# Kernel tuning notes

Hardware: AMD Instinct MI355X
Metric: run time of the kernel (lower is better)

Reference implementation:

```python
import jax, jax.numpy as jnp
import numpy as np
from jax.scipy.linalg import expm

CUTOFF = 8   # Fock cutoff D
M = 4        # qumodes
L = 2        # CVNeuralNet layers
N_OUT = 4
B = 4096     # batch
TWO_PI = 2.0 * np.pi

_n = jnp.arange(CUTOFF, dtype=jnp.float32)                      # number basis
_A = jnp.diag(jnp.sqrt(_n[1:]), 1).astype(jnp.complex64)        # annihilation op
_AD = _A.conj().T
_I = jnp.eye(CUTOFF, dtype=jnp.complex64)
_a1 = jnp.kron(_A, _I)   # mode-1 annihilation on 2-mode space
_a2 = jnp.kron(_I, _A)   # mode-2 annihilation on 2-mode space


def _disp(alpha):
    """Displacement gate D(alpha) = expm(alpha a^ - alpha* a) on truncated Fock space."""
    alpha = jnp.asarray(alpha, jnp.complex64)
    return expm(alpha * _AD - jnp.conj(alpha) * _A)


def _squeeze(r, phi):
    """Squeezing gate S(z) = expm((z* a^2 - z a^\u20202)/2), z = r e^{i phi}."""
    z = r * jnp.exp(1j * phi)
    return expm(0.5 * (jnp.conj(z) * (_A @ _A) - z * (_AD @ _AD)))


def _bs(theta, phi):
    """Beamsplitter BS(theta, phi) = expm(theta (e^{i phi} a1 a2^ - e^{-i phi} a1^ a2))."""
    H = theta * (jnp.exp(1j * phi) * _a1 @ _a2.conj().T - jnp.exp(-1j * phi) * _a1.conj().T @ _a2)
    return expm(H).reshape(CUTOFF, CUTOFF, CUTOFF, CUTOFF)


def _apply1(state, G, mode):
    # state: [B, D, D, D, D]; G: [D, D] acting on `mode`
    st = jnp.moveaxis(state, 1 + mode, -1)
    st = st @ G.T
    return jnp.moveaxis(st, -1, 1 + mode)


def _apply2(state, G, m1, m2):
    # G: [D, D, D, D] = (out1, out2, in1, in2)
    st = jnp.moveaxis(state, (1 + m1, 1 + m2), (-2, -1))
    st = jnp.einsum('ijkl,bxykl->bxyij', G, st.reshape(st.shape[0], -1, CUTOFF, CUTOFF, CUTOFF).reshape(st.shape)) if False else jnp.einsum('ijkl,b...kl->b...ij', G, st)
    return jnp.moveaxis(st, (-2, -1), (1 + m1, 1 + m2))


def _apply_diag(state, d, mode):
    shape = [1] * (M + 1)
    shape[1 + mode] = CUTOFF
    return state * d.reshape(shape)


def _interferometer(state, theta, phi, varphi):
    # PennyLane rectangular mesh: BS on (k, k+1) when (l + k) % 2 != 1, then rotations
    idx = 0
    for l in range(M):
        for k in range(M - 1):
            if (l + k) % 2 != 1:
                state = _apply2(state, _bs(theta[idx], phi[idx]), k, k + 1)
                idx += 1
    for m in range(M):
        state = _apply_diag(state, jnp.exp(1j * varphi[m] * _n), m)
    return state


def _forward(x, theta1, phi1, varphi1, r, phi_r, theta2, phi2, varphi2, a_amp, phi_a, kappa):
    # Displacement embedding: |psi0> = prod_m D(x_m)|0>, i.e. outer product of first columns
    Gs = jax.vmap(_disp)(x.reshape(-1)).reshape(x.shape[0], M, CUTOFF, CUTOFF)
    cols = Gs[..., 0]  # [B, M, D] : D(alpha)|0>
    state = jnp.einsum('bi,bj,bk,bl->bijkl', cols[:, 0], cols[:, 1], cols[:, 2], cols[:, 3])
    for l in range(L):
        state = _interferometer(state, theta1[l], phi1[l], varphi1[l])
        for m in range(M):
            state = _apply1(state, _squeeze(r[l, m], phi_r[l, m]), m)
        state = _interferometer(state, theta2[l], phi2[l], varphi2[l])
        for m in range(M):
            state = _apply1(state, _disp(a_amp[l, m] * jnp.exp(1j * phi_a[l, m])), m)
        for m in range(M):  # Kerr: diag exp(i kappa n^2)
            state = _apply_diag(state, jnp.exp(1j * kappa[l, m] * _n ** 2), m)
    # <X_i> = <a_i + a_i^> = 2 Re <psi| a_i |psi>  (hbar = 2 SF convention)
    outs = []
    for i in range(N_OUT):
        a_psi = _apply1(state, _A, i)
        exp_a = jnp.sum(jnp.conj(state) * a_psi, axis=tuple(range(1, M + 1)))
        outs.append(2.0 * jnp.real(exp_a))
    return jnp.stack(outs, axis=-1)  # [B, N_OUT]


def setup_inputs() -> dict:
    key = jax.random.key(0)
    ks = jax.random.split(key, 10)
    Kp = M * (M - 1) // 2
    u = lambda k, shape: jax.random.uniform(k, shape, jnp.float32, 0.0, TWO_PI)
    return {
        'x': jax.random.uniform(ks[0], (B, M), jnp.float32) * 0.5,
        'theta1': u(ks[1], (L, Kp)), 'phi1': u(ks[2], (L, Kp)), 'varphi1': u(ks[3], (L, M)),
        'r': jnp.full((L, M), 0.1, jnp.float32), 'phi_r': u(ks[4], (L, M)),
        'theta2': u(ks[5], (L, Kp)), 'phi2': u(ks[6], (L, Kp)), 'varphi2': u(ks[7], (L, M)),
        'a_amp': jnp.full((L, M), 0.1, jnp.float32), 'phi_a': u(ks[8], (L, M)),
        'kappa': u(ks[9], (L, M)),
    }


def reference(x, theta1, phi1, varphi1, r, phi_r, theta2, phi2, varphi2, a_amp, phi_a, kappa):
    return _forward(x, theta1, phi1, varphi1, r, phi_r, theta2, phi2, varphi2, a_amp, phi_a, kappa)
```

## Files before the change

### kernel.cpp

```cpp
#include <hip/hip_runtime.h>
#include <math.h>

#define WS_G1_OFF   (24*384)

typedef float v2f __attribute__((ext_vector_type(2)));
typedef float v4f __attribute__((ext_vector_type(4)));

__device__ __forceinline__ void cmac_s(v2f& acc, v2f s, v2f g){
  asm("v_pk_fma_f32 %0, %1, %2, %0 op_sel_hi:[0,1,1]\n\t"
      "v_pk_fma_f32 %0, %1, %2, %0 op_sel:[1,1,0] op_sel_hi:[1,0,1] neg_lo:[1,0,0]"
      : "+v"(acc) : "v"(s), "s"(g));
}
__device__ __forceinline__ v2f cmul_s0(v2f s, v2f g){
  v2f acc;
  asm("v_pk_fma_f32 %0, %1, %2, 0 op_sel_hi:[0,1,1]\n\t"
      "v_pk_fma_f32 %0, %1, %2, %0 op_sel:[1,1,0] op_sel_hi:[1,0,1] neg_lo:[1,0,0]"
      : "=&v"(acc) : "v"(s), "s"(g));
  return acc;
}
__device__ __forceinline__ void cmac_v(v2f& acc, v2f s, v2f g){
  asm("v_pk_fma_f32 %0, %1, %2, %0 op_sel_hi:[0,1,1]\n\t"
      "v_pk_fma_f32 %0, %1, %2, %0 op_sel:[1,1,0] op_sel_hi:[1,0,1] neg_lo:[1,0,0]"
      : "+v"(acc) : "v"(s), "v"(g));
}

__global__ __launch_bounds__(256) void setup_bs(
    const float* __restrict__ th1, const float* __restrict__ ph1,
    const float* __restrict__ th2, const float* __restrict__ ph2,
    float2* __restrict__ ws)
{
  __shared__ float2 bufA[4096];
  __shared__ float2 bufB[4096];
  const int g = blockIdx.x;
  const int t = threadIdx.x;
  const int l = g/12, intf = (g%12)/6, pos = g%6;
  const float th = (intf ? th2 : th1)[l*6+pos];
  const float ph = (intf ? ph2 : ph1)[l*6+pos];
  float nrm = fabsf(th)*14.0f;
  int sq = 0;
  if (nrm > 2.0f) sq = (int)ceilf(log2f(nrm*0.5f));
  const float tc  = th * ldexpf(1.0f, -sq);
  const float cph = cosf(ph), sph = sinf(ph);

  float2* cur = bufA; float2* nxt = bufB;
  for (int e=0;e<16;e++){ int idx=e*256+t;
    cur[idx] = make_float2(((idx>>6)==(idx&63))?1.f:0.f, 0.f); }
  __syncthreads();
  for (int k=12;k>=1;k--){
    const float inv = 1.0f/(float)k;
    for (int e=0;e<16;e++){
      const int idx=e*256+t; const int row=idx>>6, c=idx&63;
      const int m1=row>>3, m2=row&7;
      float vx=0.f, vy=0.f;
      if (m1<7 && m2>=1){
        const float mag = tc*sqrtf((float)((m1+1)*m2));
        const float2 q = cur[((m1+1)*8+(m2-1))*64 + c];
        vx += mag*(cph*q.x - sph*q.y);
        vy += mag*(cph*q.y + sph*q.x);
      }
      if (m1>=1 && m2<7){
        const float mag = tc*sqrtf((float)(m1*(m2+1)));
        const float2 q = cur[((m1-1)*8+(m2+1))*64 + c];
        vx -= mag*(cph*q.x + sph*q.y);
        vy -= mag*(cph*q.y - sph*q.x);
      }
      vx *= inv; vy *= inv;
      if (row==c) vx += 1.0f;
      nxt[idx] = make_float2(vx,vy);
    }
    __syncthreads();
    float2* tmp=cur; cur=nxt; nxt=tmp;
  }
  for (int si=0; si<sq; si++){
    for (int e=0;e<16;e++){
      const int idx=e*256+t; const int row=idx>>6, c=idx&63;
      const float2* Arow = cur + row*64;
      v2f acc = (v2f){0.f,0.f};
      for (int q=0;q<64;q+=2){
        const v4f ap = *(const v4f*)&Arow[q];
        const v2f b0 = *(const v2f*)&cur[q*64+c];
        const v2f b1 = *(const v2f*)&cur[(q+1)*64+c];
        cmac_v(acc, b0, (v2f){ap.x,ap.y});
        cmac_v(acc, b1, (v2f){ap.z,ap.w});
      }
      nxt[idx] = make_float2(acc.x, acc.y);
    }
    __syncthreads();
    float2* tmp=cur; cur=nxt; nxt=tmp;
  }
  for (int e=t; e<384; e+=256){
    int rem = e, N = 0, S_=0, SR_=0;
    for (; N<15; N++){
      S_  = 8 - ((N<7)?(7-N):(N-7));
      SR_ = (S_+1)&~1;
      if (rem < S_*SR_) break;
      rem -= S_*SR_;
    }
    float2 v = make_float2(0.f,0.f);
    if (N < 15){
      const int o = rem / SR_, ti = rem % SR_;
      if (ti < S_){
        const int T0 = (N>7)?(N-7):0;
        const int j = 7*(T0+o)+N, k = 7*(T0+ti)+N;
        v = cur[j*64 + k];
      }
    }
    ws[g*384 + e] = v;
  }
}

__global__ __launch_bounds__(128) void setup_small(
    const float* __restrict__ rr,  const float* __restrict__ phr,
    const float* __restrict__ aa,  const float* __restrict__ pha,
    const float* __restrict__ vph1,const float* __restrict__ vph2,
    const float* __restrict__ kap,
    float2* __restrict__ ws_g1)
{
  const int g = blockIdx.x, t = threadIdx.x;
  __shared__ float2 h8[64], bufA[64], bufB[64];
  const int isSq = (g < 8);
  const int gi = isSq ? g : (g-8);
  const int li = gi>>2, m = gi&3;
  const float p1 = isSq ? rr[li*4+m]  : aa[li*4+m];
  const float p2 = isSq ? phr[li*4+m] : pha[li*4+m];
  const float nrm = fabsf(p1)*6.0f;
  int sq = 0; if (nrm > 2.0f) sq = (int)ceilf(log2f(nrm*0.5f));
  const float sc = ldexpf(1.0f,-sq);
  const float cp = cosf(p2), sp = sinf(p2);
  if (t < 64){
    const int row=t>>3, c=t&7;
    float2 v = make_float2(0.f,0.f);
    if (isSq){
      if (c == row+2){ const float mg = 0.5f*p1*sqrtf((float)((row+1)*(row+2)));
                       v = make_float2( mg*cp, -mg*sp); }
      else if (c+2 == row){ const float mg = 0.5f*p1*sqrtf((float)((row-1)*row));
                       v = make_float2(-mg*cp, -mg*sp); }
    } else {
      if (c+1 == row){ const float mg = p1*sqrtf((float)row);
                       v = make_float2( mg*cp,  mg*sp); }
      else if (c == row+1){ const float mg = p1*sqrtf((float)(row+1));
                       v = make_float2(-mg*cp,  mg*sp); }
    }
    h8[t]   = make_float2(v.x*sc, v.y*sc);
    bufA[t] = make_float2((row==c)?1.f:0.f, 0.f);
  }
  __syncthreads();
  float2* cur=bufA; float2* nxt=bufB;
  for (int k=12;k>=1;k--){
    const float inv = 1.0f/(float)k;
    if (t<64){
      const int row=t>>3, c=t&7;
      float vx=0.f, vy=0.f;
      for (int q=0;q<8;q++){
        const float2 a_=h8[row*8+q], b_=cur[q*8+c];
        vx += a_.x*b_.x - a_.y*b_.y; vy += a_.x*b_.y + a_.y*b_.x;
      }
      vx*=inv; vy*=inv; if (row==c) vx += 1.f;
      nxt[t]=make_float2(vx,vy);
    }
    __syncthreads();
    float2* tmp=cur; cur=nxt; nxt=tmp;
  }
  for (int si=0; si<sq; si++){
    if (t<64){
      const int row=t>>3, c=t&7;
      float vx=0.f, vy=0.f;
      for (int q=0;q<8;q++){
        const float2 a_=cur[row*8+q], b_=cur[q*8+c];
        vx += a_.x*b_.x - a_.y*b_.y; vy += a_.x*b_.y + a_.y*b_.x;
      }
      nxt[t]=make_float2(vx,vy);
    }
    __syncthreads();
    float2* tmp=cur; cur=nxt; nxt=tmp;
  }
  if (t<64){
    const int kk=t>>3, j=t&7;
    const float2 v = cur[j*8+kk];
    float ang;
    if (isSq) ang = vph1[li*4+m]*(float)kk;
    else      ang = vph2[li*4+m]*(float)kk + kap[li*4+m]*(float)(j*j);
    const float ca = cosf(ang), sa = sinf(ang);
    ws_g1[g*64 + t] = make_float2(v.x*ca - v.y*sa, v.x*sa + v.y*ca);
  }
}


template<int PM>
__device__ __forceinline__ constexpr int koff(int k){
  return (PM==0) ? 65*k : ((PM==1) ? (8*k + (k>>3)) : k);
}

template<int NN,int PM>
__device__ __forceinline__ void bs_sector(const float2* __restrict__ gsec,
                                          float2* __restrict__ Sm, int sb)
{
  constexpr int S_ = 8 - ((NN<7)?(7-NN):(NN-7));
  constexpr int T0 = (NN>7)?(NN-7):0;
  constexpr int SR = (S_+1)&~1;
  v2f sv[S_];
#pragma unroll
  for (int i=0;i<S_;i++)
    sv[i] = *(const v2f*)&Sm[sb + koff<PM>(7*(T0+i)+NN)];
#pragma unroll
  for (int o=0;o<S_;o++){
    v2f acc = cmul_s0(sv[0], *(const v2f*)&gsec[o*SR]);
#pragma unroll
    for (int i=1;i<S_;i++)
      cmac_s(acc, sv[i], *(const v2f*)&gsec[o*SR+i]);
    *(v2f*)&Sm[sb + koff<PM>(7*(T0+o)+NN)] = acc;
  }
}

template<int PM>
__device__ __forceinline__ void bs_gate(const float2* __restrict__ gb,
                                        float2* __restrict__ Sm, int sb, int wvu)
{
  if (wvu==0){
    bs_sector<7 ,PM>(gb+156, Sm, sb);
    bs_sector<3 ,PM>(gb+18,  Sm, sb);
    bs_sector<13,PM>(gb+370, Sm, sb);
    bs_sector<0 ,PM>(gb+0,   Sm, sb);
  } else if (wvu==1){
    bs_sector<6 ,PM>(gb+100, Sm, sb);
    bs_sector<4 ,PM>(gb+34,  Sm, sb);
    bs_sector<2 ,PM>(gb+6,   Sm, sb);
    bs_sector<14,PM>(gb+374, Sm, sb);
  } else if (wvu==2){
    bs_sector<8 ,PM>(gb+220, Sm, sb);
    bs_sector<10,PM>(gb+312, Sm, sb);
    bs_sector<12,PM>(gb+358, Sm, sb);
    bs_sector<1 ,PM>(gb+2,   Sm, sb);
  } else {
    bs_sector<5 ,PM>(gb+64,  Sm, sb);
    bs_sector<9 ,PM>(gb+276, Sm, sb);
    bs_sector<11,PM>(gb+342, Sm, sb);
  }
  __syncthreads();
}

template<int M>
__device__ __forceinline__ void one_mode(const float2* __restrict__ gb,
                                         float2* __restrict__ Sm, int t)
{
  constexpr int ek = (M==0)?520:((M==1)?65:((M==2)?8:1));
  int base[2];
#pragma unroll
  for (int vv=0; vv<2; vv++){
    const int v = t + vv*256;
    if constexpr (M==0)      base[vv] = 65*(v>>6) + 8*((v>>3)&7) + (v&7);
    else if constexpr (M==1) base[vv] = 520*(v>>6) + 8*((v>>3)&7) + (v&7);
    else if constexpr (M==2) base[vv] = 520*(((v>>3)&1)|(((v>>7)&3)<<1)) + 65*((v>>4)&7) + (v&7);
    else                     base[vv] = 520*((v>>4)&7) + 65*(v&7) + 8*(((v>>3)&1)|(((v>>7)&3)<<1));
  }
  v2f acc[2][8];
#pragma unroll
  for (int k=0;k<8;k++){
    const v2f sA = *(const v2f*)&Sm[base[0] + ek*k];
    const v2f sB = *(const v2f*)&Sm[base[1] + ek*k];
#pragma unroll
    for (int j=0;j<8;j++){
      const v2f g = *(const v2f*)&gb[k*8+j];
      if (k==0){ acc[0][j] = cmul_s0(sA, g); acc[1][j] = cmul_s0(sB, g); }
      else     { cmac_s(acc[0][j], sA, g);   cmac_s(acc[1][j], sB, g); }
    }
  }
#pragma unroll
  for (int vv=0; vv<2; vv++)
#pragma unroll
    for (int j=0;j<8;j++) *(v2f*)&Sm[base[vv] + ek*j] = acc[vv][j];
  __syncthreads();
}

__global__ __launch_bounds__(256,4) void qnn_main(
    const float* __restrict__ x, const float2* __restrict__ ws,
    float* __restrict__ out)
{
  __shared__ __align__(16) float2 S[4160];
  __shared__ float colf[32];
  __shared__ float red[16];
  const int b = blockIdx.x, t = threadIdx.x;
  const int lane = t & 63;
  const int wvu = __builtin_amdgcn_readfirstlane(t>>6);
  const int i2c = (t>>3)&7, i3c = t&7;

  if (t < 32){
    const int m = t>>3, n = t&7;
    const float xv = x[b*4+m];
    float val = expf(-0.5f*xv*xv);
    for (int q=1;q<=n;q++) val *= xv * rsqrtf((float)q);
    colf[t] = val;
  }
  __syncthreads();
  {
    const float c23 = colf[16+i2c]*colf[24+i3c];
    const float c1a = colf[8+wvu], c1b = colf[12+wvu];
#pragma unroll
    for (int e=0;e<16;e++){
      const int idx = e*256 + t;
      const float v = colf[e>>1] * ((e&1)?c1b:c1a) * c23;
      S[idx + (idx>>6)] = make_float2(v, 0.f);
    }
  }
  __syncthreads();

  const int sbP0 = lane;
  const int sbP1 = 520*(lane>>3) + (lane&7);
  const int sbP2 = 520*(lane>>3) + 65*(lane&7);
  const float2* ws_g1 = ws + WS_G1_OFF;

#pragma unroll 1
  for (int seg=0; seg<4; seg++){
    const float2* bsg = ws + seg*(6*384);
#pragma unroll 1
    for (int q=0; q<6; q++){
      const float2* gq = bsg + q*384;
      const int pm = (q>=3)? (q-3) : q;
      if (pm==0)      bs_gate<0>(gq, S, sbP0, wvu);
      else if (pm==1) bs_gate<2>(gq, S, sbP2, wvu);
      else            bs_gate<1>(gq, S, sbP1, wvu);
    }
    const int l = seg>>1, r = seg&1;
    const float2* om = ws_g1 + (r*8 + l*4)*64;
    one_mode<0>(om,     S, t);
    one_mode<1>(om+64,  S, t);
    one_mode<2>(om+128, S, t);
    one_mode<3>(om+192, S, t);
  }

  const float w1a = sqrtf((float)(wvu+1));
  const float w1b = sqrtf((float)(wvu+5));
  const float w2 = sqrtf((float)(i2c+1)), w3 = sqrtf((float)(i3c+1));
  float am0=0.f, am1=0.f, am2=0.f, am3=0.f;
#pragma unroll
  for (int e=0;e<16;e++){
    const int idx = e*256 + t;
    const float2 a = S[idx + (idx>>6)];
    if ((e>>1) < 7){
      const int j2 = idx + 512; const float2 bz = S[j2 + (j2>>6)];
      am0 = fmaf(a.x*bz.x + a.y*bz.y, sqrtf((float)((e>>1)+1)), am0);
    }
    if (((e&1)==0) || (wvu<3)){
      const int j2 = idx + 64; const float2 bz = S[j2 + (j2>>6)];
      am1 = fmaf(a.x*bz.x + a.y*bz.y, (e&1)?w1b:w1a, am1);
    }
    if (i2c < 7){
      const int j2 = idx + 8; const float2 bz = S[j2 + (j2>>6)];
      am2 = fmaf(a.x*bz.x + a.y*bz.y, w2, am2);
    }
    if (i3c < 7){
      const int j2 = idx + 1; const float2 bz = S[j2 + (j2>>6)];
      am3 = fmaf(a.x*bz.x + a.y*bz.y, w3, am3);
    }
  }
#pragma unroll
  for (int o=32;o;o>>=1){
    am0 += __shfl_down(am0,o,64);
    am1 += __shfl_down(am1,o,64);
    am2 += __shfl_down(am2,o,64);
    am3 += __shfl_down(am3,o,64);
  }
  __syncthreads();
  if ((t&63)==0){
    red[wvu*4+0]=am0; red[wvu*4+1]=am1; red[wvu*4+2]=am2; red[wvu*4+3]=am3;
  }
  __syncthreads();
  if (t<4) out[b*4+t] = 2.f*(red[t]+red[4+t]+red[8+t]+red[12+t]);
}

extern "C" void kernel_launch(void* const* d_in, const int* in_sizes, int n_in,
                              void* d_out, int out_size, void* d_ws, size_t ws_size,
                              hipStream_t stream)
{
  const float* x    = (const float*)d_in[0];
  const float* th1  = (const float*)d_in[1];
  const float* ph1  = (const float*)d_in[2];
  const float* vph1 = (const float*)d_in[3];
  const float* rr   = (const float*)d_in[4];
  const float* phr  = (const float*)d_in[5];
  const float* th2  = (const float*)d_in[6];
  const float* ph2  = (const float*)d_in[7];
  const float* vph2 = (const float*)d_in[8];
  const float* aa   = (const float*)d_in[9];
  const float* pha  = (const float*)d_in[10];
  const float* kap  = (const float*)d_in[11];
  float2* ws  = (float2*)d_ws;
  float*  out = (float*)d_out;
  const int B = in_sizes[0] / 4;

  hipLaunchKernelGGL(setup_bs, dim3(24), dim3(256), 0, stream, th1, ph1, th2, ph2, ws);
  hipLaunchKernelGGL(setup_small, dim3(16), dim3(128), 0, stream,
                     rr, phr, aa, pha, vph1, vph2, kap, ws + WS_G1_OFF);
  hipLaunchKernelGGL(qnn_main, dim3(B), dim3(256), 0, stream, x, ws, out);
}
```

Measured before the change: 519.4 us.

## Double block size to 512 threads and redistribute beamsplitter sectors across 8 waves

Moves each batch element's block from 256 to 512 threads, so every thread handles one state column instead of two in the single-mode gates, init and measurement. The 15 photon-number sectors of each beamsplitter are rebalanced across 8 wavefronts instead of 4. The aim is more parallelism per block and shorter per-wave critical paths in the beamsplitter phase, traded for lower per-thread ILP, more threads idling at each barrier, and launch bounds that now allow only 2 blocks per CU.

Result: faster. 485.8 us, median of 2 (-6.5%).

```diff
diff --git a/kernel.cpp b/kernel.cpp
--- a/kernel.cpp
+++ b/kernel.cpp
@@ -218,22 +218,26 @@
 {
   if (wvu==0){
     bs_sector<7 ,PM>(gb+156, Sm, sb);
-    bs_sector<3 ,PM>(gb+18,  Sm, sb);
-    bs_sector<13,PM>(gb+370, Sm, sb);
-    bs_sector<0 ,PM>(gb+0,   Sm, sb);
   } else if (wvu==1){
     bs_sector<6 ,PM>(gb+100, Sm, sb);
-    bs_sector<4 ,PM>(gb+34,  Sm, sb);
-    bs_sector<2 ,PM>(gb+6,   Sm, sb);
     bs_sector<14,PM>(gb+374, Sm, sb);
   } else if (wvu==2){
     bs_sector<8 ,PM>(gb+220, Sm, sb);
+    bs_sector<0 ,PM>(gb+0,   Sm, sb);
+  } else if (wvu==3){
+    bs_sector<5 ,PM>(gb+64,  Sm, sb);
+    bs_sector<13,PM>(gb+370, Sm, sb);
+  } else if (wvu==4){
+    bs_sector<9 ,PM>(gb+276, Sm, sb);
+    bs_sector<1 ,PM>(gb+2,   Sm, sb);
+  } else if (wvu==5){
+    bs_sector<4 ,PM>(gb+34,  Sm, sb);
+    bs_sector<12,PM>(gb+358, Sm, sb);
+  } else if (wvu==6){
     bs_sector<10,PM>(gb+312, Sm, sb);
-    bs_sector<12,PM>(gb+358, Sm, sb);
-    bs_sector<1 ,PM>(gb+2,   Sm, sb);
+    bs_sector<2 ,PM>(gb+6,   Sm, sb);
   } else {
-    bs_sector<5 ,PM>(gb+64,  Sm, sb);
-    bs_sector<9 ,PM>(gb+276, Sm, sb);
+    bs_sector<3 ,PM>(gb+18,  Sm, sb);
     bs_sector<11,PM>(gb+342, Sm, sb);
   }
   __syncthreads();
@@ -244,41 +248,35 @@
                                          float2* __restrict__ Sm, int t)
 {
   constexpr int ek = (M==0)?520:((M==1)?65:((M==2)?8:1));
-  int base[2];
-#pragma unroll
-  for (int vv=0; vv<2; vv++){
-    const int v = t + vv*256;
-    if constexpr (M==0)      base[vv] = 65*(v>>6) + 8*((v>>3)&7) + (v&7);
-    else if constexpr (M==1) base[vv] = 520*(v>>6) + 8*((v>>3)&7) + (v&7);
-    else if constexpr (M==2) base[vv] = 520*(((v>>3)&1)|(((v>>7)&3)<<1)) + 65*((v>>4)&7) + (v&7);
-    else                     base[vv] = 520*((v>>4)&7) + 65*(v&7) + 8*(((v>>3)&1)|(((v>>7)&3)<<1));
-  }
-  v2f acc[2][8];
+  const int v = t;
+  int base;
+  if constexpr (M==0)      base = 65*(v>>6) + 8*((v>>3)&7) + (v&7);
+  else if constexpr (M==1) base = 520*(v>>6) + 8*((v>>3)&7) + (v&7);
+  else if constexpr (M==2) base = 520*(((v>>3)&1)|(((v>>7)&3)<<1)) + 65*((v>>4)&7) + (v&7);
+  else                     base = 520*((v>>4)&7) + 65*(v&7) + 8*(((v>>3)&1)|(((v>>7)&3)<<1));
+  v2f acc[8];
 #pragma unroll
   for (int k=0;k<8;k++){
-    const v2f sA = *(const v2f*)&Sm[base[0] + ek*k];
-    const v2f sB = *(const v2f*)&Sm[base[1] + ek*k];
+    const v2f sA = *(const v2f*)&Sm[base + ek*k];
 #pragma unroll
     for (int j=0;j<8;j++){
       const v2f g = *(const v2f*)&gb[k*8+j];
-      if (k==0){ acc[0][j] = cmul_s0(sA, g); acc[1][j] = cmul_s0(sB, g); }
-      else     { cmac_s(acc[0][j], sA, g);   cmac_s(acc[1][j], sB, g); }
-    }
-  }
-#pragma unroll
-  for (int vv=0; vv<2; vv++)
-#pragma unroll
-    for (int j=0;j<8;j++) *(v2f*)&Sm[base[vv] + ek*j] = acc[vv][j];
-  __syncthreads();
-}
-
-__global__ __launch_bounds__(256,4) void qnn_main(
+      if (k==0) acc[j] = cmul_s0(sA, g);
+      else      cmac_s(acc[j], sA, g);
+    }
+  }
+#pragma unroll
+  for (int j=0;j<8;j++) *(v2f*)&Sm[base + ek*j] = acc[j];
+  __syncthreads();
+}
+
+__global__ __launch_bounds__(512,2) void qnn_main(
     const float* __restrict__ x, const float2* __restrict__ ws,
     float* __restrict__ out)
 {
   __shared__ __align__(16) float2 S[4160];
   __shared__ float colf[32];
-  __shared__ float red[16];
+  __shared__ float red[32];
   const int b = blockIdx.x, t = threadIdx.x;
   const int lane = t & 63;
   const int wvu = __builtin_amdgcn_readfirstlane(t>>6);
@@ -294,12 +292,11 @@
   __syncthreads();
   {
     const float c23 = colf[16+i2c]*colf[24+i3c];
-    const float c1a = colf[8+wvu], c1b = colf[12+wvu];
-#pragma unroll
-    for (int e=0;e<16;e++){
-      const int idx = e*256 + t;
-      const float v = colf[e>>1] * ((e&1)?c1b:c1a) * c23;
-      S[idx + (idx>>6)] = make_float2(v, 0.f);
+    const float c1  = colf[8+wvu];
+#pragma unroll
+    for (int e=0;e<8;e++){
+      const int idx = e*512 + t;
+      S[idx + (idx>>6)] = make_float2(colf[e] * c1 * c23, 0.f);
     }
   }
   __syncthreads();
@@ -328,21 +325,20 @@
     one_mode<3>(om+192, S, t);
   }
 
-  const float w1a = sqrtf((float)(wvu+1));
-  const float w1b = sqrtf((float)(wvu+5));
+  const float w1 = sqrtf((float)(wvu+1));
   const float w2 = sqrtf((float)(i2c+1)), w3 = sqrtf((float)(i3c+1));
   float am0=0.f, am1=0.f, am2=0.f, am3=0.f;
 #pragma unroll
-  for (int e=0;e<16;e++){
-    const int idx = e*256 + t;
+  for (int e=0;e<8;e++){
+    const int idx = e*512 + t;
     const float2 a = S[idx + (idx>>6)];
-    if ((e>>1) < 7){
+    if (e < 7){
       const int j2 = idx + 512; const float2 bz = S[j2 + (j2>>6)];
-      am0 = fmaf(a.x*bz.x + a.y*bz.y, sqrtf((float)((e>>1)+1)), am0);
-    }
-    if (((e&1)==0) || (wvu<3)){
+      am0 = fmaf(a.x*bz.x + a.y*bz.y, sqrtf((float)(e+1)), am0);
+    }
+    if (wvu < 7){
       const int j2 = idx + 64; const float2 bz = S[j2 + (j2>>6)];
-      am1 = fmaf(a.x*bz.x + a.y*bz.y, (e&1)?w1b:w1a, am1);
+      am1 = fmaf(a.x*bz.x + a.y*bz.y, w1, am1);
     }
     if (i2c < 7){
       const int j2 = idx + 8; const float2 bz = S[j2 + (j2>>6)];
@@ -365,7 +361,12 @@
     red[wvu*4+0]=am0; red[wvu*4+1]=am1; red[wvu*4+2]=am2; red[wvu*4+3]=am3;
   }
   __syncthreads();
-  if (t<4) out[b*4+t] = 2.f*(red[t]+red[4+t]+red[8+t]+red[12+t]);
+  if (t<4){
+    float s = 0.f;
+#pragma unroll
+    for (int w=0;w<8;w++) s += red[w*4+t];
+    out[b*4+t] = 2.f*s;
+  }
 }
 
 extern "C" void kernel_launch(void* const* d_in, const int* in_sizes, int n_in,
@@ -391,5 +392,5 @@
   hipLaunchKernelGGL(setup_bs, dim3(24), dim3(256), 0, stream, th1, ph1, th2, ph2, ws);
   hipLaunchKernelGGL(setup_small, dim3(16), dim3(128), 0, stream,
                      rr, phr, aa, pha, vph1, vph2, kap, ws + WS_G1_OFF);
-  hipLaunchKernelGGL(qnn_main, dim3(B), dim3(256), 0, stream, x, ws, out);
-}
+  hipLaunchKernelGGL(qnn_main, dim3(B), dim3(512), 0, stream, x, ws, out);
+}
```
